# Optimization experiments

Measured on AMD Instinct MI355X. Metric: run time of the kernel, lower is better.

Reference implementation:

```python
import jax, jax.numpy as jnp
import numpy as np

I = 256  # input size
H = 256  # hidden size
B = 128
S = 1024
EPS = 1e-5


def setup_inputs() -> dict:
    key = jax.random.key(0)
    ks = jax.random.split(key, 8)
    bound = 1.0 / np.sqrt(H)
    x = jax.random.normal(ks[0], (B, S, I), dtype=jnp.float32)
    mask = jax.random.randint(ks[1], (B, S), 0, 2) == 1
    W_ih = jax.random.uniform(ks[2], (4 * H, I), jnp.float32, -bound, bound)
    W_hh = jax.random.uniform(ks[3], (4 * H, H), jnp.float32, -bound, bound)
    b_ih = jax.random.uniform(ks[4], (4 * H,), jnp.float32, -bound, bound)
    b_hh = jax.random.uniform(ks[5], (4 * H,), jnp.float32, -bound, bound)
    gamma = jnp.ones((H,), jnp.float32)
    beta = jnp.zeros((H,), jnp.float32)
    return {"x": x, "mask": mask, "W_ih": W_ih, "W_hh": W_hh,
            "b_ih": b_ih, "b_hh": b_hh, "gamma": gamma, "beta": beta}


def _layernorm(h, gamma, beta):
    mu = jnp.mean(h, axis=-1, keepdims=True)
    var = jnp.var(h, axis=-1, keepdims=True)
    return (h - mu) * jax.lax.rsqrt(var + EPS) * gamma + beta


def reference(x, mask, W_ih, W_hh, b_ih, b_hh, gamma, beta):
    b = x.shape[0]
    h0 = jnp.zeros((b, H), x.dtype)
    c0 = jnp.zeros((b, H), x.dtype)
    out0 = jnp.zeros((b, H), x.dtype)

    def step(carry, inp):
        h, c, out = carry
        x_t, m_t = inp  # (B,I), (B,)
        hn = _layernorm(h, gamma, beta)
        gates = x_t @ W_ih.T + b_ih + hn @ W_hh.T + b_hh  # (B,4H)
        i_g, f_g, g_g, o_g = jnp.split(gates, 4, axis=-1)
        c = jax.nn.sigmoid(f_g) * c + jax.nn.sigmoid(i_g) * jnp.tanh(g_g)
        h = jax.nn.sigmoid(o_g) * jnp.tanh(c)
        # output[~mask] = h[~mask]; where mask is True the old output is kept
        out = jnp.where(m_t[:, None], out, h)
        return (h, c, out), None

    xs = (jnp.swapaxes(x, 0, 1), jnp.swapaxes(mask, 0, 1))  # (S,B,I), (S,B)
    (h, c, out), _ = jax.lax.scan(step, (h0, c0, out0), xs)
    return out
```

## Files before the change

kernel.cpp:

```cpp
#include <hip/hip_runtime.h>
#include <hip/hip_bf16.h>
#include <stdint.h>


#define Bb 128
#define Ss 1024
#define Ii 256
#define Hh 256
#define G4v 1024
#define EPSF 1e-5f

typedef __bf16 bf16;
typedef _Float16 f16;
typedef __attribute__((ext_vector_type(8))) __bf16 bf16x8;
typedef __attribute__((ext_vector_type(4))) __bf16 bf16x4;
typedef __attribute__((ext_vector_type(8))) _Float16 f16x8;
typedef __attribute__((ext_vector_type(4))) _Float16 f16x4;
typedef __attribute__((ext_vector_type(4))) float f32x4;
typedef unsigned int u32;
typedef unsigned long long u64;

static __device__ __forceinline__ f32x4 mfma16b(bf16x8 a, bf16x8 b, f32x4 c) {
  return __builtin_amdgcn_mfma_f32_16x16x32_bf16(a, b, c, 0, 0, 0);
}
static __device__ __forceinline__ f32x4 mfma16h(f16x8 a, f16x8 b, f32x4 c) {
  return __builtin_amdgcn_mfma_f32_16x16x32_f16(a, b, c, 0, 0, 0);
}
static __device__ __forceinline__ float sigm(float x) { return 1.0f / (1.0f + __expf(-x)); }
static __device__ __forceinline__ float tanhf_(float x) {
  float e = __expf(-2.0f * fabsf(x));
  float t = (1.0f - e) / (1.0f + e);
  return x < 0.0f ? -t : t;
}
static __device__ __forceinline__ unsigned short ush(f16 h) {
  return __builtin_bit_cast(unsigned short, h);
}
static __device__ __forceinline__ f16 hus(unsigned short u) {
  return __builtin_bit_cast(f16, u);
}

__global__ void k_conv_wih(const float* __restrict__ W, bf16* __restrict__ hi,
                           bf16* __restrict__ lo) {
  int i = (blockIdx.x * 256 + threadIdx.x) * 4;
  f32x4 v = *(const f32x4*)(W + i);
  bf16x4 h_, l_;
#pragma unroll
  for (int j = 0; j < 4; ++j) {
    bf16 hh = (bf16)v[j];
    h_[j] = hh;
    l_[j] = (bf16)(v[j] - (float)hh);
  }
  *(bf16x4*)(hi + i) = h_;
  *(bf16x4*)(lo + i) = l_;
}

__global__ void k_prep_whh(const float* __restrict__ W, const float* __restrict__ gamma,
                           f16* __restrict__ Wf) {
  int tid = blockIdx.x * 256 + threadIdx.x;
  int lane = tid & 63;
  int fk = tid >> 6;
  int ntg = fk >> 3, kt = fk & 7;
  int g = ntg * 16 + (lane & 15);
  int k = kt * 32 + ((lane >> 4) << 3);
  f16x8 r;
#pragma unroll
  for (int j = 0; j < 8; ++j) r[j] = (f16)(W[g * Hh + k + j] * gamma[k + j]);
  *(f16x8*)(Wf + (size_t)tid * 8) = r;
}

__global__ void k_prep_rd(const float* __restrict__ W, const float* __restrict__ gamma,
                          const float* __restrict__ beta, const float* __restrict__ bih,
                          const float* __restrict__ bhh, float* __restrict__ RD) {
  int g = blockIdx.x * 256 + threadIdx.x;
  float r = 0.f, d = 0.f;
  for (int k = 0; k < Hh; ++k) {
    float w = W[g * Hh + k];
    r += w * gamma[k];
    d += w * beta[k];
  }
  RD[2 * g] = r;
  RD[2 * g + 1] = d + bih[g] + bhh[g];
}

__global__ __launch_bounds__(256, 2) void k_gemm(const float* __restrict__ x,
                                                 const bf16* __restrict__ Whi,
                                                 const bf16* __restrict__ Wlo,
                                                 float* __restrict__ xw,
                                                 int t0, int Tc, int ntb) {
  __shared__ bf16 Bs[2][128 * 128];
  int bid = blockIdx.x;
  int b = bid & 127;
  int r2 = bid >> 7;
  int tb = r2 % ntb;
  int gt = r2 / ntb;
  int g0 = gt * 128;
  int tid = threadIdx.x, w = tid >> 6, lane = tid & 63;
  int li = lane & 15, lg = lane >> 4;
  char* BsB = (char*)Bs;
  int tbase = tb * 128 + 32 * w;
  f32x4 acc[2][8];
#pragma unroll
  for (int mt = 0; mt < 2; ++mt)
#pragma unroll
    for (int nt = 0; nt < 8; ++nt) acc[mt][nt] = (f32x4){0.f, 0.f, 0.f, 0.f};

  for (int kp = 0; kp < 2; ++kp) {
#pragma unroll
    for (int it = 0; it < 8; ++it) {
      int p = it * 4096 + tid * 16;
      int row = p >> 8, colb = p & 255;
      size_t goff = (size_t)(g0 + row) * 512 + kp * 256 + colb;
      int dst = row * 256 + (colb ^ ((row & 7) << 4));
      *(bf16x8*)(BsB + dst) = *(const bf16x8*)((const char*)Whi + goff);
      *(bf16x8*)(BsB + 32768 + dst) = *(const bf16x8*)((const char*)Wlo + goff);
    }
    __syncthreads();
#pragma unroll
    for (int kt = 0; kt < 4; ++kt) {
      int kl = kt * 32 + lg * 8;
      int kgl = kp * 128 + kl;
      bf16x8 ah[2], al[2];
#pragma unroll
      for (int mt = 0; mt < 2; ++mt) {
        int t = t0 + tbase + 16 * mt + li;
        const float* xp = x + ((size_t)b * Ss + t) * Ii + kgl;
        f32x4 f0 = *(const f32x4*)xp;
        f32x4 f1 = *(const f32x4*)(xp + 4);
        bf16x8 hv, lv;
#pragma unroll
        for (int j = 0; j < 4; ++j) {
          bf16 h0 = (bf16)f0[j];
          hv[j] = h0;
          lv[j] = (bf16)(f0[j] - (float)h0);
          bf16 h1 = (bf16)f1[j];
          hv[4 + j] = h1;
          lv[4 + j] = (bf16)(f1[j] - (float)h1);
        }
        ah[mt] = hv;
        al[mt] = lv;
      }
#pragma unroll
      for (int nt = 0; nt < 8; ++nt) {
        int grow = nt * 16 + li;
        int off = grow * 256 + ((kl * 2) ^ ((grow & 7) << 4));
        bf16x8 bh = *(const bf16x8*)(BsB + off);
        bf16x8 bl = *(const bf16x8*)(BsB + 32768 + off);
#pragma unroll
        for (int mt = 0; mt < 2; ++mt) {
          acc[mt][nt] = mfma16b(ah[mt], bh, acc[mt][nt]);
          acc[mt][nt] = mfma16b(ah[mt], bl, acc[mt][nt]);
          acc[mt][nt] = mfma16b(al[mt], bh, acc[mt][nt]);
        }
      }
    }
    __syncthreads();
  }
#pragma unroll
  for (int mt = 0; mt < 2; ++mt)
#pragma unroll
    for (int nt = 0; nt < 8; ++nt)
#pragma unroll
      for (int r = 0; r < 4; ++r) {
        int tl = tbase + 16 * mt + lg * 4 + r;
        int g = g0 + nt * 16 + li;
        xw[((size_t)b * Tc + tl) * G4v + g] = acc[mt][nt][r];
      }
}

__global__ __launch_bounds__(256, 1) void k_recur(
    const f16* __restrict__ Wf, const float* __restrict__ xw,
    const int* __restrict__ mask, const float* __restrict__ RD,
    float* __restrict__ st_h, float* __restrict__ st_c, float* __restrict__ st_o,
    u64* pub, float* __restrict__ out, int t0, int Tc, int first, int last) {
  __shared__ f16 hb[2][16 * 256];
  __shared__ float murs[2][16][2];
  __shared__ float2 spw[4][16];
  __shared__ float spart[16][16][2];
  int bid = blockIdx.x;
  int grp = bid & 7, q = bid >> 3;
  int tid = threadIdx.x, w = tid >> 6, lane = tid & 63;
  int li = lane & 15, lg = lane >> 4;
  int b0 = grp * 16;
  int jloc = (q * 4 + w) * 16 + li;
  char* hbB = (char*)hb;

  f16x8 wp[4][8];
#pragma unroll
  for (int c = 0; c < 4; ++c)
#pragma unroll
    for (int kt = 0; kt < 8; ++kt) {
      int ntg = c * 16 + q * 4 + w;
      wp[c][kt] = *(const f16x8*)(Wf + ((size_t)(ntg * 8 + kt) * 64 + lane) * 8);
      asm volatile("" : "+a"(wp[c][kt]));
    }
  float Rr[4], Dd[4];
#pragma unroll
  for (int c = 0; c < 4; ++c) {
    int g = c * 256 + jloc;
    Rr[c] = RD[2 * g];
    Dd[c] = RD[2 * g + 1];
  }

  float cst[4], ost[4];
  if (first) {
#pragma unroll
    for (int i = 0; i < 16; ++i) {
      hb[0][tid * 16 + i] = (f16)0.0f;
      hb[1][tid * 16 + i] = (f16)0.0f;
    }
#pragma unroll
    for (int r = 0; r < 4; ++r) { cst[r] = 0.f; ost[r] = 0.f; }
    if (tid < 16) { murs[0][tid][0] = 0.f; murs[0][tid][1] = rsqrtf(EPSF); }
  } else {
    int row = tid >> 4, cs = tid & 15, jseg = cs * 16;
    float s = 0.f, ss = 0.f;
#pragma unroll
    for (int i = 0; i < 16; ++i) {
      float v = st_h[(size_t)(b0 + row) * Hh + jseg + i];
      s += v;
      ss += v * v;
      f16 hh = (f16)v;
      int boff = row * 512 + (((jseg + i) * 2) ^ ((row & 7) << 4));
      *(f16*)(hbB + boff) = hh;
      *(f16*)(hbB + 8192 + boff) = (f16)(v - (float)hh);
    }
    spart[row][cs][0] = s;
    spart[row][cs][1] = ss;
#pragma unroll
    for (int r = 0; r < 4; ++r) {
      int m = lg * 4 + r;
      cst[r] = st_c[(size_t)(b0 + m) * Hh + jloc];
      ost[r] = st_o[(size_t)(b0 + m) * Hh + jloc];
    }
    __syncthreads();
    if (tid < 16) {
      float s2 = 0.f, ss2 = 0.f;
#pragma unroll
      for (int i = 0; i < 16; ++i) { s2 += spart[tid][i][0]; ss2 += spart[tid][i][1]; }
      float mu = s2 * (1.f / 256.f);
      float var = ss2 * (1.f / 256.f) - mu * mu;
      float rs = rsqrtf(var + EPSF);
      murs[0][tid][0] = mu * rs;
      murs[0][tid][1] = rs;
    }
  }
  __syncthreads();

  float xwv[4][4];
  int mk[4];
#pragma unroll
  for (int c = 0; c < 4; ++c)
#pragma unroll
    for (int r = 0; r < 4; ++r)
      xwv[c][r] = xw[((size_t)(b0 + lg * 4 + r) * Tc + 0) * G4v + c * 256 + jloc];
#pragma unroll
  for (int r = 0; r < 4; ++r) mk[r] = mask[(size_t)(b0 + lg * 4 + r) * Ss + t0];

  int grow = tid >> 4, gcg = tid & 15;

  for (int tl = 0; tl < Tc; ++tl) {
    int tg = t0 + tl;
    int slot = (tg + 1) & 1;
    u32 want = (u32)(tg + 1);

    f32x4 a0[4], a1[4];
#pragma unroll
    for (int c = 0; c < 4; ++c) {
      a0[c] = (f32x4){0.f, 0.f, 0.f, 0.f};
      a1[c] = (f32x4){0.f, 0.f, 0.f, 0.f};
    }
#pragma unroll
    for (int kt = 0; kt < 8; ++kt) {
      int aoff = li * 512 + (((kt * 32 + lg * 8) * 2) ^ ((li & 7) << 4));
      f16x8 ah = *(const f16x8*)(hbB + aoff);
      f16x8 al = *(const f16x8*)(hbB + 8192 + aoff);
#pragma unroll
      for (int c = 0; c < 4; ++c) {
        a0[c] = mfma16h(ah, wp[c][kt], a0[c]);
        a1[c] = mfma16h(al, wp[c][kt], a1[c]);
      }
    }
    float mrs[4], rsv[4];
#pragma unroll
    for (int r = 0; r < 4; ++r) {
      int m = lg * 4 + r;
      mrs[r] = murs[tl & 1][m][0];
      rsv[r] = murs[tl & 1][m][1];
    }
    __syncthreads();

    float hnew[4];
#pragma unroll
    for (int r = 0; r < 4; ++r) {
      float i_ = (a0[0][r] + a1[0][r]) * rsv[r] - mrs[r] * Rr[0] + Dd[0] + xwv[0][r];
      float f_ = (a0[1][r] + a1[1][r]) * rsv[r] - mrs[r] * Rr[1] + Dd[1] + xwv[1][r];
      float g_ = (a0[2][r] + a1[2][r]) * rsv[r] - mrs[r] * Rr[2] + Dd[2] + xwv[2][r];
      float o_ = (a0[3][r] + a1[3][r]) * rsv[r] - mrs[r] * Rr[3] + Dd[3] + xwv[3][r];
      float cn = sigm(f_) * cst[r] + sigm(i_) * tanhf_(g_);
      float hn = sigm(o_) * tanhf_(cn);
      cst[r] = cn;
      ost[r] = mk[r] ? ost[r] : hn;
      hnew[r] = hn;
    }
    u64* ph = pub + (size_t)(slot * 32 + bid) * 1024;
#pragma unroll
    for (int r = 0; r < 4; ++r) {
      int m = lg * 4 + r;
      float hn = hnew[r];
      f16 hh = (f16)hn;
      f16 hl = (f16)(hn - (float)hh);
      int boff = m * 512 + ((jloc * 2) ^ ((m & 7) << 4));
      *(f16*)(hbB + boff) = hh;
      *(f16*)(hbB + 8192 + boff) = hl;
      u64 pv = ((u64)want << 32) | ((u32)ush(hh) << 16) | (u32)ush(hl);
      __hip_atomic_store(&ph[m * 64 + (w * 16 + li)], pv, __ATOMIC_RELAXED,
                         __HIP_MEMORY_SCOPE_AGENT);
    }

    u64 gv[3][4];
    const u64* srcs[3];
#pragma unroll
    for (int pi = 0; pi < 3; ++pi) {
      int qq = (q + 1 + pi) & 3;
      int pbid = qq * 8 + grp;
      srcs[pi] = pub + (size_t)(slot * 32 + pbid) * 1024 + grow * 64 + gcg * 4;
#pragma unroll
      for (int e = 0; e < 4; ++e)
        gv[pi][e] = __hip_atomic_load(&srcs[pi][e], __ATOMIC_RELAXED,
                                      __HIP_MEMORY_SCOPE_AGENT);
    }

    {
      float sr[4], qr[4];
#pragma unroll
      for (int r = 0; r < 4; ++r) { sr[r] = hnew[r]; qr[r] = hnew[r] * hnew[r]; }
#pragma unroll
      for (int msk = 1; msk < 16; msk <<= 1)
#pragma unroll
        for (int r = 0; r < 4; ++r) {
          sr[r] += __shfl_xor(sr[r], msk);
          qr[r] += __shfl_xor(qr[r], msk);
        }
      if (li == 0)
#pragma unroll
        for (int r = 0; r < 4; ++r) spw[w][lg * 4 + r] = make_float2(sr[r], qr[r]);
    }
    if (tl == Tc - 1) {
#pragma unroll
      for (int r = 0; r < 4; ++r) {
        int m = lg * 4 + r;
        st_h[(size_t)(b0 + m) * Hh + jloc] = hnew[r];
        st_c[(size_t)(b0 + m) * Hh + jloc] = cst[r];
        st_o[(size_t)(b0 + m) * Hh + jloc] = ost[r];
      }
      if (last) {
#pragma unroll
        for (int r = 0; r < 4; ++r) out[(size_t)(b0 + lg * 4 + r) * Hh + jloc] = ost[r];
      }
    }
    {
      int tln = (tl + 1 < Tc) ? tl + 1 : Tc - 1;
#pragma unroll
      for (int c = 0; c < 4; ++c)
#pragma unroll
        for (int r = 0; r < 4; ++r)
          xwv[c][r] = xw[((size_t)(b0 + lg * 4 + r) * Tc + tln) * G4v + c * 256 + jloc];
#pragma unroll
      for (int r = 0; r < 4; ++r) mk[r] = mask[(size_t)(b0 + lg * 4 + r) * Ss + t0 + tln];
    }

    {
      u32 bad = 0;
#pragma unroll
      for (int pi = 0; pi < 3; ++pi)
#pragma unroll
        for (int e = 0; e < 4; ++e) bad |= (u32)(gv[pi][e] >> 32) ^ want;
      int cnt = 0;
      while (bad) {
#pragma unroll
        for (int pi = 0; pi < 3; ++pi)
#pragma unroll
          for (int e = 0; e < 4; ++e)
            gv[pi][e] = __hip_atomic_load(&srcs[pi][e], __ATOMIC_RELAXED,
                                          __HIP_MEMORY_SCOPE_AGENT);
        bad = 0;
#pragma unroll
        for (int pi = 0; pi < 3; ++pi)
#pragma unroll
          for (int e = 0; e < 4; ++e) bad |= (u32)(gv[pi][e] >> 32) ^ want;
        if (++cnt > (1 << 20)) break;
      }
    }
    float su = 0.f, qu = 0.f;
#pragma unroll
    for (int pi = 0; pi < 3; ++pi) {
      int qq = (q + 1 + pi) & 3;
      int j0 = qq * 64 + gcg * 4;
      int boff = grow * 512 + ((j0 * 2) ^ ((grow & 7) << 4));
      f16x4 h4, l4;
#pragma unroll
      for (int e = 0; e < 4; ++e) {
        u32 d = (u32)gv[pi][e];
        f16 hh = hus((unsigned short)(d >> 16));
        f16 hl = hus((unsigned short)(d & 0xffffu));
        h4[e] = hh;
        l4[e] = hl;
        float f = (float)hh + (float)hl;
        su += f;
        qu += f * f;
      }
      *(f16x4*)(hbB + boff) = h4;
      *(f16x4*)(hbB + 8192 + boff) = l4;
    }
#pragma unroll
    for (int msk = 1; msk < 16; msk <<= 1) {
      su += __shfl_xor(su, msk);
      qu += __shfl_xor(qu, msk);
    }
    __syncthreads();
    if (li == 0) {
      float s = su + spw[0][grow].x + spw[1][grow].x + spw[2][grow].x + spw[3][grow].x;
      float ss2 = qu + spw[0][grow].y + spw[1][grow].y + spw[2][grow].y + spw[3][grow].y;
      float mu = s * (1.f / 256.f);
      float var = ss2 * (1.f / 256.f) - mu * mu;
      float rs = rsqrtf(var + EPSF);
      murs[(tl + 1) & 1][grow][0] = mu * rs;
      murs[(tl + 1) & 1][grow][1] = rs;
    }
  }
}

extern "C" void kernel_launch(void* const* d_in, const int* in_sizes, int n_in,
                              void* d_out, int out_size, void* d_ws, size_t ws_size,
                              hipStream_t stream) {
  (void)in_sizes; (void)n_in; (void)out_size;
  const float* x = (const float*)d_in[0];
  const int* mask = (const int*)d_in[1];
  const float* Wih = (const float*)d_in[2];
  const float* Whh = (const float*)d_in[3];
  const float* bih = (const float*)d_in[4];
  const float* bhh = (const float*)d_in[5];
  const float* gamma = (const float*)d_in[6];
  const float* beta = (const float*)d_in[7];
  float* outp = (float*)d_out;
  char* ws = (char*)d_ws;

  const size_t extra = 3 * (512u << 10) + (8u << 10) + 3 * (128u << 10) +
                       (512u << 10) + (64u << 10);
  int Tc = 128;
  if (ws_size >= (size_t)1024 * 524288 + extra) Tc = 1024;
  else if (ws_size >= (size_t)512 * 524288 + extra) Tc = 512;
  else if (ws_size >= (size_t)256 * 524288 + extra) Tc = 256;

  size_t o = 0;
  auto take = [&](size_t bytes) { size_t r = o; o += (bytes + 255) & ~(size_t)255; return r; };
  size_t xw_off = take((size_t)Bb * Tc * G4v * 4);
  size_t wihh_off = take(512u << 10);
  size_t wihl_off = take(512u << 10);
  size_t whh_off = take(512u << 10);
  size_t rd_off = take(8u << 10);
  size_t sth_off = take(128u << 10);
  size_t stc_off = take(128u << 10);
  size_t sto_off = take(128u << 10);
  size_t pub_off = take(512u << 10);

  bf16* wihh = (bf16*)(ws + wihh_off);
  bf16* wihl = (bf16*)(ws + wihl_off);
  f16* whhf = (f16*)(ws + whh_off);
  float* rd = (float*)(ws + rd_off);
  float* xwp = (float*)(ws + xw_off);
  float* sth = (float*)(ws + sth_off);
  float* stc = (float*)(ws + stc_off);
  float* sto = (float*)(ws + sto_off);
  u64* pubh = (u64*)(ws + pub_off);

  hipMemsetAsync(pubh, 0, 512u << 10, stream);
  k_conv_wih<<<dim3(256), dim3(256), 0, stream>>>(Wih, wihh, wihl);
  k_prep_whh<<<dim3(128), dim3(256), 0, stream>>>(Whh, gamma, whhf);
  k_prep_rd<<<dim3(4), dim3(256), 0, stream>>>(Whh, gamma, beta, bih, bhh, rd);

  int nchunk = Ss / Tc;
  int ntb = Tc / 128;
  for (int ci = 0; ci < nchunk; ++ci) {
    int t0 = ci * Tc;
    k_gemm<<<dim3(8 * ntb * 128), dim3(256), 0, stream>>>(x, wihh, wihl, xwp, t0, Tc, ntb);
    k_recur<<<dim3(32), dim3(256), 0, stream>>>(whhf, xwp, mask, rd, sth, stc, sto,
                                                pubh, outp, t0, Tc,
                                                ci == 0 ? 1 : 0, ci == nchunk - 1 ? 1 : 0);
  }
}
```

Baseline: 4.757 ms.

## Give each recurrent block a full hidden slice, removing cross-block spin synchronization

The recurrence now runs on 8 workgroups, each owning 16 batch rows and all 256 hidden units. Previously 32 workgroups split the hidden dimension and exchanged h every step through atomic publish/poll in global memory, with a spin wait. Now each step needs only block-local barriers and LDS. Each workgroup does four times the MFMA work per step, so the recurrent weights are split three ways: half held in registers, a quarter staged in dynamic LDS, and a quarter re-read from global/L2 every step. This trades per-step inter-block latency for more per-block compute and weight traffic.

```diff
diff --git a/kernel.cpp b/kernel.cpp
--- a/kernel.cpp
+++ b/kernel.cpp
@@ -10,15 +10,21 @@
 #define G4v 1024
 #define EPSF 1e-5f
 
+#define OFF_W 0
+#define OFF_HBH 131072
+#define OFF_HBL 139264
+#define OFF_RD 147456
+#define OFF_MURS 155648
+#define OFF_SPW 155904
+#define OFF_SPART 156416
+#define LDS_TOTAL 158464
+
 typedef __bf16 bf16;
 typedef _Float16 f16;
 typedef __attribute__((ext_vector_type(8))) __bf16 bf16x8;
-typedef __attribute__((ext_vector_type(4))) __bf16 bf16x4;
 typedef __attribute__((ext_vector_type(8))) _Float16 f16x8;
-typedef __attribute__((ext_vector_type(4))) _Float16 f16x4;
 typedef __attribute__((ext_vector_type(4))) float f32x4;
 typedef unsigned int u32;
-typedef unsigned long long u64;
 
 static __device__ __forceinline__ f32x4 mfma16b(bf16x8 a, bf16x8 b, f32x4 c) {
   return __builtin_amdgcn_mfma_f32_16x16x32_bf16(a, b, c, 0, 0, 0);
@@ -32,26 +38,17 @@
   float t = (1.0f - e) / (1.0f + e);
   return x < 0.0f ? -t : t;
 }
-static __device__ __forceinline__ unsigned short ush(f16 h) {
-  return __builtin_bit_cast(unsigned short, h);
-}
-static __device__ __forceinline__ f16 hus(unsigned short u) {
-  return __builtin_bit_cast(f16, u);
-}
 
 __global__ void k_conv_wih(const float* __restrict__ W, bf16* __restrict__ hi,
                            bf16* __restrict__ lo) {
   int i = (blockIdx.x * 256 + threadIdx.x) * 4;
   f32x4 v = *(const f32x4*)(W + i);
-  bf16x4 h_, l_;
 #pragma unroll
   for (int j = 0; j < 4; ++j) {
     bf16 hh = (bf16)v[j];
-    h_[j] = hh;
-    l_[j] = (bf16)(v[j] - (float)hh);
-  }
-  *(bf16x4*)(hi + i) = h_;
-  *(bf16x4*)(lo + i) = l_;
+    hi[i + j] = hh;
+    lo[i + j] = (bf16)(v[j] - (float)hh);
+  }
 }
 
 __global__ void k_prep_whh(const float* __restrict__ W, const float* __restrict__ gamma,
@@ -171,46 +168,58 @@
     const f16* __restrict__ Wf, const float* __restrict__ xw,
     const int* __restrict__ mask, const float* __restrict__ RD,
     float* __restrict__ st_h, float* __restrict__ st_c, float* __restrict__ st_o,
-    u64* pub, float* __restrict__ out, int t0, int Tc, int first, int last) {
-  __shared__ f16 hb[2][16 * 256];
-  __shared__ float murs[2][16][2];
-  __shared__ float2 spw[4][16];
-  __shared__ float spart[16][16][2];
+    float* __restrict__ out, int t0, int Tc, int first, int last) {
+  extern __shared__ char smem[];
+  char* WldsB = smem + OFF_W;
+  char* hbH = smem + OFF_HBH;
+  char* hbL = smem + OFF_HBL;
+  float* rdl = (float*)(smem + OFF_RD);
+  float(*murs)[16][2] = (float(*)[16][2])(smem + OFF_MURS);
+  float2(*spw)[16] = (float2(*)[16])(smem + OFF_SPW);
+  float(*spart)[16][2] = (float(*)[16][2])(smem + OFF_SPART);
+
   int bid = blockIdx.x;
-  int grp = bid & 7, q = bid >> 3;
   int tid = threadIdx.x, w = tid >> 6, lane = tid & 63;
   int li = lane & 15, lg = lane >> 4;
-  int b0 = grp * 16;
-  int jloc = (q * 4 + w) * 16 + li;
-  char* hbB = (char*)hb;
-
-  f16x8 wp[4][8];
+  int b0 = bid * 16;
+
+  f16x8 wp[2][4][8];
+#pragma unroll
+  for (int jt = 0; jt < 2; ++jt)
+#pragma unroll
+    for (int c = 0; c < 4; ++c)
+#pragma unroll
+      for (int kt = 0; kt < 8; ++kt) {
+        int ntg = c * 16 + (w * 4 + jt);
+        wp[jt][c][kt] = *(const f16x8*)(Wf + ((size_t)(ntg * 8 + kt) * 64 + lane) * 8);
+        asm volatile("" : "+a"(wp[jt][c][kt]));
+      }
 #pragma unroll
   for (int c = 0; c < 4; ++c)
 #pragma unroll
     for (int kt = 0; kt < 8; ++kt) {
-      int ntg = c * 16 + q * 4 + w;
-      wp[c][kt] = *(const f16x8*)(Wf + ((size_t)(ntg * 8 + kt) * 64 + lane) * 8);
-      asm volatile("" : "+a"(wp[c][kt]));
-    }
-  float Rr[4], Dd[4];
-#pragma unroll
-  for (int c = 0; c < 4; ++c) {
-    int g = c * 256 + jloc;
-    Rr[c] = RD[2 * g];
-    Dd[c] = RD[2 * g + 1];
-  }
-
-  float cst[4], ost[4];
+      int ntg = c * 16 + (w * 4 + 2);
+      f16x8 v = *(const f16x8*)(Wf + ((size_t)(ntg * 8 + kt) * 64 + lane) * 8);
+      *(f16x8*)(WldsB + (size_t)((w * 32 + c * 8 + kt) * 64 + lane) * 16) = v;
+    }
+  *(f32x4*)(rdl + tid * 8) = *(const f32x4*)(RD + tid * 8);
+  *(f32x4*)(rdl + tid * 8 + 4) = *(const f32x4*)(RD + tid * 8 + 4);
+
+  float cst[4][4], ost[4][4];
   if (first) {
 #pragma unroll
     for (int i = 0; i < 16; ++i) {
-      hb[0][tid * 16 + i] = (f16)0.0f;
-      hb[1][tid * 16 + i] = (f16)0.0f;
-    }
-#pragma unroll
-    for (int r = 0; r < 4; ++r) { cst[r] = 0.f; ost[r] = 0.f; }
-    if (tid < 16) { murs[0][tid][0] = 0.f; murs[0][tid][1] = rsqrtf(EPSF); }
+      ((f16*)hbH)[tid * 16 + i] = (f16)0.0f;
+      ((f16*)hbL)[tid * 16 + i] = (f16)0.0f;
+    }
+#pragma unroll
+    for (int jt = 0; jt < 4; ++jt)
+#pragma unroll
+      for (int r = 0; r < 4; ++r) { cst[jt][r] = 0.f; ost[jt][r] = 0.f; }
+    if (tid < 16) {
+      murs[0][tid][0] = 0.f;
+      murs[0][tid][1] = rsqrtf(EPSF);
+    }
   } else {
     int row = tid >> 4, cs = tid & 15, jseg = cs * 16;
     float s = 0.f, ss = 0.f;
@@ -221,16 +230,20 @@
       ss += v * v;
       f16 hh = (f16)v;
       int boff = row * 512 + (((jseg + i) * 2) ^ ((row & 7) << 4));
-      *(f16*)(hbB + boff) = hh;
-      *(f16*)(hbB + 8192 + boff) = (f16)(v - (float)hh);
+      *(f16*)(hbH + boff) = hh;
+      *(f16*)(hbL + boff) = (f16)(v - (float)hh);
     }
     spart[row][cs][0] = s;
     spart[row][cs][1] = ss;
 #pragma unroll
-    for (int r = 0; r < 4; ++r) {
-      int m = lg * 4 + r;
-      cst[r] = st_c[(size_t)(b0 + m) * Hh + jloc];
-      ost[r] = st_o[(size_t)(b0 + m) * Hh + jloc];
+    for (int jt = 0; jt < 4; ++jt) {
+      int jloc = (w * 4 + jt) * 16 + li;
+#pragma unroll
+      for (int r = 0; r < 4; ++r) {
+        int m = lg * 4 + r;
+        cst[jt][r] = st_c[(size_t)(b0 + m) * Hh + jloc];
+        ost[jt][r] = st_o[(size_t)(b0 + m) * Hh + jloc];
+      }
     }
     __syncthreads();
     if (tid < 16) {
@@ -246,40 +259,39 @@
   }
   __syncthreads();
 
-  float xwv[4][4];
   int mk[4];
 #pragma unroll
-  for (int c = 0; c < 4; ++c)
-#pragma unroll
-    for (int r = 0; r < 4; ++r)
-      xwv[c][r] = xw[((size_t)(b0 + lg * 4 + r) * Tc + 0) * G4v + c * 256 + jloc];
-#pragma unroll
   for (int r = 0; r < 4; ++r) mk[r] = mask[(size_t)(b0 + lg * 4 + r) * Ss + t0];
 
-  int grow = tid >> 4, gcg = tid & 15;
-
   for (int tl = 0; tl < Tc; ++tl) {
-    int tg = t0 + tl;
-    int slot = (tg + 1) & 1;
-    u32 want = (u32)(tg + 1);
-
-    f32x4 a0[4], a1[4];
-#pragma unroll
-    for (int c = 0; c < 4; ++c) {
-      a0[c] = (f32x4){0.f, 0.f, 0.f, 0.f};
-      a1[c] = (f32x4){0.f, 0.f, 0.f, 0.f};
-    }
+    f16x8 ah[8], al[8];
 #pragma unroll
     for (int kt = 0; kt < 8; ++kt) {
       int aoff = li * 512 + (((kt * 32 + lg * 8) * 2) ^ ((li & 7) << 4));
-      f16x8 ah = *(const f16x8*)(hbB + aoff);
-      f16x8 al = *(const f16x8*)(hbB + 8192 + aoff);
-#pragma unroll
-      for (int c = 0; c < 4; ++c) {
-        a0[c] = mfma16h(ah, wp[c][kt], a0[c]);
-        a1[c] = mfma16h(al, wp[c][kt], a1[c]);
-      }
-    }
+      ah[kt] = *(const f16x8*)(hbH + aoff);
+      al[kt] = *(const f16x8*)(hbL + aoff);
+    }
+    float xwc[4][4];
+    {
+      int jl0 = (w * 4) * 16 + li;
+#pragma unroll
+      for (int c = 0; c < 4; ++c)
+#pragma unroll
+        for (int r = 0; r < 4; ++r)
+          xwc[c][r] = xw[((size_t)(b0 + lg * 4 + r) * Tc + tl) * G4v + c * 256 + jl0];
+    }
+    f16x8 wsA[8], wsB[8];
+#pragma unroll
+    for (int kt = 0; kt < 8; ++kt) {
+      int ntg = 0 * 16 + (w * 4 + 3);
+      wsA[kt] = *(const f16x8*)(Wf + ((size_t)(ntg * 8 + kt) * 64 + lane) * 8);
+    }
+    int tln = (tl + 1 < Tc) ? tl + 1 : Tc - 1;
+    int mkn[4];
+#pragma unroll
+    for (int r = 0; r < 4; ++r) mkn[r] = mask[(size_t)(b0 + lg * 4 + r) * Ss + t0 + tln];
+
+    __syncthreads();
     float mrs[4], rsv[4];
 #pragma unroll
     for (int r = 0; r < 4; ++r) {
@@ -287,145 +299,124 @@
       mrs[r] = murs[tl & 1][m][0];
       rsv[r] = murs[tl & 1][m][1];
     }
+    float sr[4] = {0.f, 0.f, 0.f, 0.f}, qr[4] = {0.f, 0.f, 0.f, 0.f};
+    int lastStep = (tl == Tc - 1);
+
+#pragma unroll
+    for (int jt = 0; jt < 4; ++jt) {
+      int jloc = (w * 4 + jt) * 16 + li;
+      float xwn[4][4];
+      if (jt < 3) {
+        int jln = (w * 4 + jt + 1) * 16 + li;
+#pragma unroll
+        for (int c = 0; c < 4; ++c)
+#pragma unroll
+          for (int r = 0; r < 4; ++r)
+            xwn[c][r] = xw[((size_t)(b0 + lg * 4 + r) * Tc + tl) * G4v + c * 256 + jln];
+      }
+      f32x4 acc[4];
+#pragma unroll
+      for (int c = 0; c < 4; ++c) acc[c] = (f32x4){0.f, 0.f, 0.f, 0.f};
+      if (jt < 2) {
+#pragma unroll
+        for (int c = 0; c < 4; ++c)
+#pragma unroll
+          for (int kt = 0; kt < 8; ++kt) {
+            acc[c] = mfma16h(ah[kt], wp[jt][c][kt], acc[c]);
+            acc[c] = mfma16h(al[kt], wp[jt][c][kt], acc[c]);
+          }
+      } else if (jt == 2) {
+#pragma unroll
+        for (int c = 0; c < 4; ++c) {
+          f16x8 wl[8];
+#pragma unroll
+          for (int kt = 0; kt < 8; ++kt)
+            wl[kt] = *(const f16x8*)(WldsB +
+                                     (size_t)((w * 32 + c * 8 + kt) * 64 + lane) * 16);
+#pragma unroll
+          for (int kt = 0; kt < 8; ++kt) {
+            acc[c] = mfma16h(ah[kt], wl[kt], acc[c]);
+            acc[c] = mfma16h(al[kt], wl[kt], acc[c]);
+          }
+        }
+      } else {
+#pragma unroll
+        for (int c = 0; c < 4; ++c) {
+          if (c < 3) {
+            int ntg = (c + 1) * 16 + (w * 4 + 3);
+#pragma unroll
+            for (int kt = 0; kt < 8; ++kt) {
+              f16x8 v = *(const f16x8*)(Wf + ((size_t)(ntg * 8 + kt) * 64 + lane) * 8);
+              if (c & 1) wsA[kt] = v; else wsB[kt] = v;
+            }
+          }
+#pragma unroll
+          for (int kt = 0; kt < 8; ++kt) {
+            f16x8 wc = (c & 1) ? wsB[kt] : wsA[kt];
+            acc[c] = mfma16h(ah[kt], wc, acc[c]);
+            acc[c] = mfma16h(al[kt], wc, acc[c]);
+          }
+        }
+      }
+      float Rrc[4], Ddc[4];
+#pragma unroll
+      for (int c = 0; c < 4; ++c) {
+        int g = c * 256 + jloc;
+        Rrc[c] = rdl[2 * g];
+        Ddc[c] = rdl[2 * g + 1];
+      }
+#pragma unroll
+      for (int r = 0; r < 4; ++r) {
+        float i_ = acc[0][r] * rsv[r] - mrs[r] * Rrc[0] + Ddc[0] + xwc[0][r];
+        float f_ = acc[1][r] * rsv[r] - mrs[r] * Rrc[1] + Ddc[1] + xwc[1][r];
+        float g_ = acc[2][r] * rsv[r] - mrs[r] * Rrc[2] + Ddc[2] + xwc[2][r];
+        float o_ = acc[3][r] * rsv[r] - mrs[r] * Rrc[3] + Ddc[3] + xwc[3][r];
+        float cn = sigm(f_) * cst[jt][r] + sigm(i_) * tanhf_(g_);
+        float hn = sigm(o_) * tanhf_(cn);
+        cst[jt][r] = cn;
+        ost[jt][r] = mk[r] ? ost[jt][r] : hn;
+        int m = lg * 4 + r;
+        int boff = m * 512 + ((jloc * 2) ^ ((m & 7) << 4));
+        f16 hh = (f16)hn;
+        *(f16*)(hbH + boff) = hh;
+        *(f16*)(hbL + boff) = (f16)(hn - (float)hh);
+        sr[r] += hn;
+        qr[r] += hn * hn;
+        if (lastStep) {
+          st_h[(size_t)(b0 + m) * Hh + jloc] = hn;
+          st_c[(size_t)(b0 + m) * Hh + jloc] = cst[jt][r];
+          st_o[(size_t)(b0 + m) * Hh + jloc] = ost[jt][r];
+          if (last) out[(size_t)(b0 + m) * Hh + jloc] = ost[jt][r];
+        }
+      }
+      if (jt < 3) {
+#pragma unroll
+        for (int c = 0; c < 4; ++c)
+#pragma unroll
+          for (int r = 0; r < 4; ++r) xwc[c][r] = xwn[c][r];
+      }
+    }
+#pragma unroll
+    for (int msk = 1; msk < 16; msk <<= 1)
+#pragma unroll
+      for (int r = 0; r < 4; ++r) {
+        sr[r] += __shfl_xor(sr[r], msk);
+        qr[r] += __shfl_xor(qr[r], msk);
+      }
+    if (li == 0)
+#pragma unroll
+      for (int r = 0; r < 4; ++r) spw[w][lg * 4 + r] = make_float2(sr[r], qr[r]);
+#pragma unroll
+    for (int r = 0; r < 4; ++r) mk[r] = mkn[r];
     __syncthreads();
-
-    float hnew[4];
-#pragma unroll
-    for (int r = 0; r < 4; ++r) {
-      float i_ = (a0[0][r] + a1[0][r]) * rsv[r] - mrs[r] * Rr[0] + Dd[0] + xwv[0][r];
-      float f_ = (a0[1][r] + a1[1][r]) * rsv[r] - mrs[r] * Rr[1] + Dd[1] + xwv[1][r];
-      float g_ = (a0[2][r] + a1[2][r]) * rsv[r] - mrs[r] * Rr[2] + Dd[2] + xwv[2][r];
-      float o_ = (a0[3][r] + a1[3][r]) * rsv[r] - mrs[r] * Rr[3] + Dd[3] + xwv[3][r];
-      float cn = sigm(f_) * cst[r] + sigm(i_) * tanhf_(g_);
-      float hn = sigm(o_) * tanhf_(cn);
-      cst[r] = cn;
-      ost[r] = mk[r] ? ost[r] : hn;
-      hnew[r] = hn;
-    }
-    u64* ph = pub + (size_t)(slot * 32 + bid) * 1024;
-#pragma unroll
-    for (int r = 0; r < 4; ++r) {
-      int m = lg * 4 + r;
-      float hn = hnew[r];
-      f16 hh = (f16)hn;
-      f16 hl = (f16)(hn - (float)hh);
-      int boff = m * 512 + ((jloc * 2) ^ ((m & 7) << 4));
-      *(f16*)(hbB + boff) = hh;
-      *(f16*)(hbB + 8192 + boff) = hl;
-      u64 pv = ((u64)want << 32) | ((u32)ush(hh) << 16) | (u32)ush(hl);
-      __hip_atomic_store(&ph[m * 64 + (w * 16 + li)], pv, __ATOMIC_RELAXED,
-                         __HIP_MEMORY_SCOPE_AGENT);
-    }
-
-    u64 gv[3][4];
-    const u64* srcs[3];
-#pragma unroll
-    for (int pi = 0; pi < 3; ++pi) {
-      int qq = (q + 1 + pi) & 3;
-      int pbid = qq * 8 + grp;
-      srcs[pi] = pub + (size_t)(slot * 32 + pbid) * 1024 + grow * 64 + gcg * 4;
-#pragma unroll
-      for (int e = 0; e < 4; ++e)
-        gv[pi][e] = __hip_atomic_load(&srcs[pi][e], __ATOMIC_RELAXED,
-                                      __HIP_MEMORY_SCOPE_AGENT);
-    }
-
-    {
-      float sr[4], qr[4];
-#pragma unroll
-      for (int r = 0; r < 4; ++r) { sr[r] = hnew[r]; qr[r] = hnew[r] * hnew[r]; }
-#pragma unroll
-      for (int msk = 1; msk < 16; msk <<= 1)
-#pragma unroll
-        for (int r = 0; r < 4; ++r) {
-          sr[r] += __shfl_xor(sr[r], msk);
-          qr[r] += __shfl_xor(qr[r], msk);
-        }
-      if (li == 0)
-#pragma unroll
-        for (int r = 0; r < 4; ++r) spw[w][lg * 4 + r] = make_float2(sr[r], qr[r]);
-    }
-    if (tl == Tc - 1) {
-#pragma unroll
-      for (int r = 0; r < 4; ++r) {
-        int m = lg * 4 + r;
-        st_h[(size_t)(b0 + m) * Hh + jloc] = hnew[r];
-        st_c[(size_t)(b0 + m) * Hh + jloc] = cst[r];
-        st_o[(size_t)(b0 + m) * Hh + jloc] = ost[r];
-      }
-      if (last) {
-#pragma unroll
-        for (int r = 0; r < 4; ++r) out[(size_t)(b0 + lg * 4 + r) * Hh + jloc] = ost[r];
-      }
-    }
-    {
-      int tln = (tl + 1 < Tc) ? tl + 1 : Tc - 1;
-#pragma unroll
-      for (int c = 0; c < 4; ++c)
-#pragma unroll
-        for (int r = 0; r < 4; ++r)
-          xwv[c][r] = xw[((size_t)(b0 + lg * 4 + r) * Tc + tln) * G4v + c * 256 + jloc];
-#pragma unroll
-      for (int r = 0; r < 4; ++r) mk[r] = mask[(size_t)(b0 + lg * 4 + r) * Ss + t0 + tln];
-    }
-
-    {
-      u32 bad = 0;
-#pragma unroll
-      for (int pi = 0; pi < 3; ++pi)
-#pragma unroll
-        for (int e = 0; e < 4; ++e) bad |= (u32)(gv[pi][e] >> 32) ^ want;
-      int cnt = 0;
-      while (bad) {
-#pragma unroll
-        for (int pi = 0; pi < 3; ++pi)
-#pragma unroll
-          for (int e = 0; e < 4; ++e)
-            gv[pi][e] = __hip_atomic_load(&srcs[pi][e], __ATOMIC_RELAXED,
-                                          __HIP_MEMORY_SCOPE_AGENT);
-        bad = 0;
-#pragma unroll
-        for (int pi = 0; pi < 3; ++pi)
-#pragma unroll
-          for (int e = 0; e < 4; ++e) bad |= (u32)(gv[pi][e] >> 32) ^ want;
-        if (++cnt > (1 << 20)) break;
-      }
-    }
-    float su = 0.f, qu = 0.f;
-#pragma unroll
-    for (int pi = 0; pi < 3; ++pi) {
-      int qq = (q + 1 + pi) & 3;
-      int j0 = qq * 64 + gcg * 4;
-      int boff = grow * 512 + ((j0 * 2) ^ ((grow & 7) << 4));
-      f16x4 h4, l4;
-#pragma unroll
-      for (int e = 0; e < 4; ++e) {
-        u32 d = (u32)gv[pi][e];
-        f16 hh = hus((unsigned short)(d >> 16));
-        f16 hl = hus((unsigned short)(d & 0xffffu));
-        h4[e] = hh;
-        l4[e] = hl;
-        float f = (float)hh + (float)hl;
-        su += f;
-        qu += f * f;
-      }
-      *(f16x4*)(hbB + boff) = h4;
-      *(f16x4*)(hbB + 8192 + boff) = l4;
-    }
-#pragma unroll
-    for (int msk = 1; msk < 16; msk <<= 1) {
-      su += __shfl_xor(su, msk);
-      qu += __shfl_xor(qu, msk);
-    }
-    __syncthreads();
-    if (li == 0) {
-      float s = su + spw[0][grow].x + spw[1][grow].x + spw[2][grow].x + spw[3][grow].x;
-      float ss2 = qu + spw[0][grow].y + spw[1][grow].y + spw[2][grow].y + spw[3][grow].y;
+    if (tid < 16) {
+      float s = spw[0][tid].x + spw[1][tid].x + spw[2][tid].x + spw[3][tid].x;
+      float ss2 = spw[0][tid].y + spw[1][tid].y + spw[2][tid].y + spw[3][tid].y;
       float mu = s * (1.f / 256.f);
       float var = ss2 * (1.f / 256.f) - mu * mu;
       float rs = rsqrtf(var + EPSF);
-      murs[(tl + 1) & 1][grow][0] = mu * rs;
-      murs[(tl + 1) & 1][grow][1] = rs;
+      murs[(tl + 1) & 1][tid][0] = mu * rs;
+      murs[(tl + 1) & 1][tid][1] = rs;
     }
   }
 }
@@ -445,8 +436,14 @@
   float* outp = (float*)d_out;
   char* ws = (char*)d_ws;
 
-  const size_t extra = 3 * (512u << 10) + (8u << 10) + 3 * (128u << 10) +
-                       (512u << 10) + (64u << 10);
+  static int lds_set = 0;
+  if (!lds_set) {
+    hipFuncSetAttribute((const void*)k_recur,
+                        hipFuncAttributeMaxDynamicSharedMemorySize, LDS_TOTAL);
+    lds_set = 1;
+  }
+
+  const size_t extra = 3 * (512u << 10) + (8u << 10) + 3 * (128u << 10) + (64u << 10);
   int Tc = 128;
   if (ws_size >= (size_t)1024 * 524288 + extra) Tc = 1024;
   else if (ws_size >= (size_t)512 * 524288 + extra) Tc = 512;
@@ -462,7 +459,6 @@
   size_t sth_off = take(128u << 10);
   size_t stc_off = take(128u << 10);
   size_t sto_off = take(128u << 10);
-  size_t pub_off = take(512u << 10);
 
   bf16* wihh = (bf16*)(ws + wihh_off);
   bf16* wihl = (bf16*)(ws + wihl_off);
@@ -472,9 +468,7 @@
   float* sth = (float*)(ws + sth_off);
   float* stc = (float*)(ws + stc_off);
   float* sto = (float*)(ws + sto_off);
-  u64* pubh = (u64*)(ws + pub_off);
-
-  hipMemsetAsync(pubh, 0, 512u << 10, stream);
+
   k_conv_wih<<<dim3(256), dim3(256), 0, stream>>>(Wih, wihh, wihl);
   k_prep_whh<<<dim3(128), dim3(256), 0, stream>>>(Whh, gamma, whhf);
   k_prep_rd<<<dim3(4), dim3(256), 0, stream>>>(Whh, gamma, beta, bih, bhh, rd);
@@ -484,8 +478,8 @@
   for (int ci = 0; ci < nchunk; ++ci) {
     int t0 = ci * Tc;
     k_gemm<<<dim3(8 * ntb * 128), dim3(256), 0, stream>>>(x, wihh, wihl, xwp, t0, Tc, ntb);
-    k_recur<<<dim3(32), dim3(256), 0, stream>>>(whhf, xwp, mask, rd, sth, stc, sto,
-                                                pubh, outp, t0, Tc,
-                                                ci == 0 ? 1 : 0, ci == nchunk - 1 ? 1 : 0);
-  }
-}
+    k_recur<<<dim3(8), dim3(256), LDS_TOTAL, stream>>>(whhf, xwp, mask, rd, sth, stc, sto,
+                                                       outp, t0, Tc,
+                                                       ci == 0 ? 1 : 0, ci == nchunk - 1 ? 1 : 0);
+  }
+}
```

After: 15.27 ms. 221% more time.

## Split recurrence across 16 blocks with pairwise hidden-state exchange

Applied to the files above, without the earlier changes.

The recurrent kernel now runs on 16 workgroups instead of 32. Each block owns 128 hidden units for a 16-row batch group and exchanges its half of h with a single partner block instead of three peers. This cuts per-step cross-block polling and publish traffic, and each wave now issues twice as many MFMAs from register-resident weights. The cost is more weight registers per wave, fewer CUs on the serial critical path, and an extra barrier per step. The bf16 weight conversion kernel also switches from vector stores to scalar stores.

```diff
diff --git a/kernel.cpp b/kernel.cpp
--- a/kernel.cpp
+++ b/kernel.cpp
@@ -13,9 +13,7 @@
 typedef __bf16 bf16;
 typedef _Float16 f16;
 typedef __attribute__((ext_vector_type(8))) __bf16 bf16x8;
-typedef __attribute__((ext_vector_type(4))) __bf16 bf16x4;
 typedef __attribute__((ext_vector_type(8))) _Float16 f16x8;
-typedef __attribute__((ext_vector_type(4))) _Float16 f16x4;
 typedef __attribute__((ext_vector_type(4))) float f32x4;
 typedef unsigned int u32;
 typedef unsigned long long u64;
@@ -43,15 +41,12 @@
                            bf16* __restrict__ lo) {
   int i = (blockIdx.x * 256 + threadIdx.x) * 4;
   f32x4 v = *(const f32x4*)(W + i);
-  bf16x4 h_, l_;
 #pragma unroll
   for (int j = 0; j < 4; ++j) {
     bf16 hh = (bf16)v[j];
-    h_[j] = hh;
-    l_[j] = (bf16)(v[j] - (float)hh);
-  }
-  *(bf16x4*)(hi + i) = h_;
-  *(bf16x4*)(lo + i) = l_;
+    hi[i + j] = hh;
+    lo[i + j] = (bf16)(v[j] - (float)hh);
+  }
 }
 
 __global__ void k_prep_whh(const float* __restrict__ W, const float* __restrict__ gamma,
@@ -172,44 +167,54 @@
     const int* __restrict__ mask, const float* __restrict__ RD,
     float* __restrict__ st_h, float* __restrict__ st_c, float* __restrict__ st_o,
     u64* pub, float* __restrict__ out, int t0, int Tc, int first, int last) {
-  __shared__ f16 hb[2][16 * 256];
+  __shared__ f16 hbH[16 * 256];
+  __shared__ f16 hbL[16 * 256];
   __shared__ float murs[2][16][2];
   __shared__ float2 spw[4][16];
+  __shared__ float2 sprem[16];
   __shared__ float spart[16][16][2];
   int bid = blockIdx.x;
-  int grp = bid & 7, q = bid >> 3;
+  int grp = bid & 7, half = bid >> 3;
   int tid = threadIdx.x, w = tid >> 6, lane = tid & 63;
   int li = lane & 15, lg = lane >> 4;
   int b0 = grp * 16;
-  int jloc = (q * 4 + w) * 16 + li;
-  char* hbB = (char*)hb;
-
-  f16x8 wp[4][8];
-#pragma unroll
-  for (int c = 0; c < 4; ++c)
-#pragma unroll
-    for (int kt = 0; kt < 8; ++kt) {
-      int ntg = c * 16 + q * 4 + w;
-      wp[c][kt] = *(const f16x8*)(Wf + ((size_t)(ntg * 8 + kt) * 64 + lane) * 8);
-      asm volatile("" : "+a"(wp[c][kt]));
-    }
-  float Rr[4], Dd[4];
-#pragma unroll
-  for (int c = 0; c < 4; ++c) {
-    int g = c * 256 + jloc;
-    Rr[c] = RD[2 * g];
-    Dd[c] = RD[2 * g + 1];
-  }
-
-  float cst[4], ost[4];
+  char* hbHB = (char*)hbH;
+  char* hbLB = (char*)hbL;
+
+  f16x8 wp[2][4][8];
+#pragma unroll
+  for (int jt = 0; jt < 2; ++jt)
+#pragma unroll
+    for (int c = 0; c < 4; ++c)
+#pragma unroll
+      for (int kt = 0; kt < 8; ++kt) {
+        int ntg = c * 16 + (half * 8 + w * 2 + jt);
+        wp[jt][c][kt] = *(const f16x8*)(Wf + ((size_t)(ntg * 8 + kt) * 64 + lane) * 8);
+        asm volatile("" : "+a"(wp[jt][c][kt]));
+      }
+  int jloc0 = half * 128 + (w * 2) * 16 + li;
+  int jloc1 = jloc0 + 16;
+  float Rr[2][4], Dd[2][4];
+#pragma unroll
+  for (int jt = 0; jt < 2; ++jt)
+#pragma unroll
+    for (int c = 0; c < 4; ++c) {
+      int g = c * 256 + (jt ? jloc1 : jloc0);
+      Rr[jt][c] = RD[2 * g];
+      Dd[jt][c] = RD[2 * g + 1];
+    }
+
+  float cst[2][4], ost[2][4];
   if (first) {
 #pragma unroll
     for (int i = 0; i < 16; ++i) {
-      hb[0][tid * 16 + i] = (f16)0.0f;
-      hb[1][tid * 16 + i] = (f16)0.0f;
-    }
-#pragma unroll
-    for (int r = 0; r < 4; ++r) { cst[r] = 0.f; ost[r] = 0.f; }
+      hbH[tid * 16 + i] = (f16)0.0f;
+      hbL[tid * 16 + i] = (f16)0.0f;
+    }
+#pragma unroll
+    for (int jt = 0; jt < 2; ++jt)
+#pragma unroll
+      for (int r = 0; r < 4; ++r) { cst[jt][r] = 0.f; ost[jt][r] = 0.f; }
     if (tid < 16) { murs[0][tid][0] = 0.f; murs[0][tid][1] = rsqrtf(EPSF); }
   } else {
     int row = tid >> 4, cs = tid & 15, jseg = cs * 16;
@@ -221,16 +226,20 @@
       ss += v * v;
       f16 hh = (f16)v;
       int boff = row * 512 + (((jseg + i) * 2) ^ ((row & 7) << 4));
-      *(f16*)(hbB + boff) = hh;
-      *(f16*)(hbB + 8192 + boff) = (f16)(v - (float)hh);
+      *(f16*)(hbHB + boff) = hh;
+      *(f16*)(hbLB + boff) = (f16)(v - (float)hh);
     }
     spart[row][cs][0] = s;
     spart[row][cs][1] = ss;
 #pragma unroll
-    for (int r = 0; r < 4; ++r) {
-      int m = lg * 4 + r;
-      cst[r] = st_c[(size_t)(b0 + m) * Hh + jloc];
-      ost[r] = st_o[(size_t)(b0 + m) * Hh + jloc];
+    for (int jt = 0; jt < 2; ++jt) {
+      int jl = jt ? jloc1 : jloc0;
+#pragma unroll
+      for (int r = 0; r < 4; ++r) {
+        int m = lg * 4 + r;
+        cst[jt][r] = st_c[(size_t)(b0 + m) * Hh + jl];
+        ost[jt][r] = st_o[(size_t)(b0 + m) * Hh + jl];
+      }
     }
     __syncthreads();
     if (tid < 16) {
@@ -246,40 +255,50 @@
   }
   __syncthreads();
 
-  float xwv[4][4];
+  float xwv[2][4][4];
   int mk[4];
 #pragma unroll
-  for (int c = 0; c < 4; ++c)
-#pragma unroll
-    for (int r = 0; r < 4; ++r)
-      xwv[c][r] = xw[((size_t)(b0 + lg * 4 + r) * Tc + 0) * G4v + c * 256 + jloc];
+  for (int jt = 0; jt < 2; ++jt) {
+    int jl = jt ? jloc1 : jloc0;
+#pragma unroll
+    for (int c = 0; c < 4; ++c)
+#pragma unroll
+      for (int r = 0; r < 4; ++r)
+        xwv[jt][c][r] = xw[((size_t)(b0 + lg * 4 + r) * Tc + 0) * G4v + c * 256 + jl];
+  }
 #pragma unroll
   for (int r = 0; r < 4; ++r) mk[r] = mask[(size_t)(b0 + lg * 4 + r) * Ss + t0];
 
   int grow = tid >> 4, gcg = tid & 15;
+  int phalf = half ^ 1;
+  int pbid = bid ^ 8;
 
   for (int tl = 0; tl < Tc; ++tl) {
     int tg = t0 + tl;
     int slot = (tg + 1) & 1;
     u32 want = (u32)(tg + 1);
 
-    f32x4 a0[4], a1[4];
-#pragma unroll
-    for (int c = 0; c < 4; ++c) {
-      a0[c] = (f32x4){0.f, 0.f, 0.f, 0.f};
-      a1[c] = (f32x4){0.f, 0.f, 0.f, 0.f};
-    }
+    f16x8 ah[8], al[8];
 #pragma unroll
     for (int kt = 0; kt < 8; ++kt) {
       int aoff = li * 512 + (((kt * 32 + lg * 8) * 2) ^ ((li & 7) << 4));
-      f16x8 ah = *(const f16x8*)(hbB + aoff);
-      f16x8 al = *(const f16x8*)(hbB + 8192 + aoff);
-#pragma unroll
-      for (int c = 0; c < 4; ++c) {
-        a0[c] = mfma16h(ah, wp[c][kt], a0[c]);
-        a1[c] = mfma16h(al, wp[c][kt], a1[c]);
-      }
-    }
+      ah[kt] = *(const f16x8*)(hbHB + aoff);
+      al[kt] = *(const f16x8*)(hbLB + aoff);
+    }
+    f32x4 acc[2][4];
+#pragma unroll
+    for (int jt = 0; jt < 2; ++jt)
+#pragma unroll
+      for (int c = 0; c < 4; ++c) acc[jt][c] = (f32x4){0.f, 0.f, 0.f, 0.f};
+#pragma unroll
+    for (int kt = 0; kt < 8; ++kt)
+#pragma unroll
+      for (int jt = 0; jt < 2; ++jt)
+#pragma unroll
+        for (int c = 0; c < 4; ++c) {
+          acc[jt][c] = mfma16h(ah[kt], wp[jt][c][kt], acc[jt][c]);
+          acc[jt][c] = mfma16h(al[kt], wp[jt][c][kt], acc[jt][c]);
+        }
     float mrs[4], rsv[4];
 #pragma unroll
     for (int r = 0; r < 4; ++r) {
@@ -289,82 +308,81 @@
     }
     __syncthreads();
 
-    float hnew[4];
-#pragma unroll
-    for (int r = 0; r < 4; ++r) {
-      float i_ = (a0[0][r] + a1[0][r]) * rsv[r] - mrs[r] * Rr[0] + Dd[0] + xwv[0][r];
-      float f_ = (a0[1][r] + a1[1][r]) * rsv[r] - mrs[r] * Rr[1] + Dd[1] + xwv[1][r];
-      float g_ = (a0[2][r] + a1[2][r]) * rsv[r] - mrs[r] * Rr[2] + Dd[2] + xwv[2][r];
-      float o_ = (a0[3][r] + a1[3][r]) * rsv[r] - mrs[r] * Rr[3] + Dd[3] + xwv[3][r];
-      float cn = sigm(f_) * cst[r] + sigm(i_) * tanhf_(g_);
-      float hn = sigm(o_) * tanhf_(cn);
-      cst[r] = cn;
-      ost[r] = mk[r] ? ost[r] : hn;
-      hnew[r] = hn;
-    }
-    u64* ph = pub + (size_t)(slot * 32 + bid) * 1024;
-#pragma unroll
-    for (int r = 0; r < 4; ++r) {
-      int m = lg * 4 + r;
-      float hn = hnew[r];
-      f16 hh = (f16)hn;
-      f16 hl = (f16)(hn - (float)hh);
-      int boff = m * 512 + ((jloc * 2) ^ ((m & 7) << 4));
-      *(f16*)(hbB + boff) = hh;
-      *(f16*)(hbB + 8192 + boff) = hl;
-      u64 pv = ((u64)want << 32) | ((u32)ush(hh) << 16) | (u32)ush(hl);
-      __hip_atomic_store(&ph[m * 64 + (w * 16 + li)], pv, __ATOMIC_RELAXED,
-                         __HIP_MEMORY_SCOPE_AGENT);
-    }
-
-    u64 gv[3][4];
-    const u64* srcs[3];
-#pragma unroll
-    for (int pi = 0; pi < 3; ++pi) {
-      int qq = (q + 1 + pi) & 3;
-      int pbid = qq * 8 + grp;
-      srcs[pi] = pub + (size_t)(slot * 32 + pbid) * 1024 + grow * 64 + gcg * 4;
-#pragma unroll
-      for (int e = 0; e < 4; ++e)
-        gv[pi][e] = __hip_atomic_load(&srcs[pi][e], __ATOMIC_RELAXED,
-                                      __HIP_MEMORY_SCOPE_AGENT);
-    }
-
-    {
-      float sr[4], qr[4];
-#pragma unroll
-      for (int r = 0; r < 4; ++r) { sr[r] = hnew[r]; qr[r] = hnew[r] * hnew[r]; }
-#pragma unroll
-      for (int msk = 1; msk < 16; msk <<= 1)
+    float sr[4] = {0.f, 0.f, 0.f, 0.f}, qr[4] = {0.f, 0.f, 0.f, 0.f};
+    float hnS[2][4];
+    u64* ph = pub + (size_t)(slot * 16 + bid) * 2048;
+#pragma unroll
+    for (int jt = 0; jt < 2; ++jt) {
+      int jl = jt ? jloc1 : jloc0;
+      int loc = jl - half * 128;
+#pragma unroll
+      for (int r = 0; r < 4; ++r) {
+        float i_ = acc[jt][0][r] * rsv[r] - mrs[r] * Rr[jt][0] + Dd[jt][0] + xwv[jt][0][r];
+        float f_ = acc[jt][1][r] * rsv[r] - mrs[r] * Rr[jt][1] + Dd[jt][1] + xwv[jt][1][r];
+        float g_ = acc[jt][2][r] * rsv[r] - mrs[r] * Rr[jt][2] + Dd[jt][2] + xwv[jt][2][r];
+        float o_ = acc[jt][3][r] * rsv[r] - mrs[r] * Rr[jt][3] + Dd[jt][3] + xwv[jt][3][r];
+        float cn = sigm(f_) * cst[jt][r] + sigm(i_) * tanhf_(g_);
+        float hn = sigm(o_) * tanhf_(cn);
+        cst[jt][r] = cn;
+        ost[jt][r] = mk[r] ? ost[jt][r] : hn;
+        hnS[jt][r] = hn;
+        int m = lg * 4 + r;
+        f16 hh = (f16)hn;
+        f16 hl = (f16)(hn - (float)hh);
+        int boff = m * 512 + ((jl * 2) ^ ((m & 7) << 4));
+        *(f16*)(hbHB + boff) = hh;
+        *(f16*)(hbLB + boff) = hl;
+        u64 pv = ((u64)want << 32) | ((u32)ush(hh) << 16) | (u32)ush(hl);
+        __hip_atomic_store(&ph[m * 128 + loc], pv, __ATOMIC_RELAXED,
+                           __HIP_MEMORY_SCOPE_AGENT);
+        sr[r] += hn;
+        qr[r] += hn * hn;
+      }
+    }
+
+    const u64* src = pub + (size_t)(slot * 16 + pbid) * 2048 + grow * 128 + gcg * 8;
+    u64 gv[8];
+#pragma unroll
+    for (int e = 0; e < 8; ++e)
+      gv[e] = __hip_atomic_load(&src[e], __ATOMIC_RELAXED, __HIP_MEMORY_SCOPE_AGENT);
+
+#pragma unroll
+    for (int msk = 1; msk < 16; msk <<= 1)
+#pragma unroll
+      for (int r = 0; r < 4; ++r) {
+        sr[r] += __shfl_xor(sr[r], msk);
+        qr[r] += __shfl_xor(qr[r], msk);
+      }
+    if (li == 0)
+#pragma unroll
+      for (int r = 0; r < 4; ++r) spw[w][lg * 4 + r] = make_float2(sr[r], qr[r]);
+
+    if (tl == Tc - 1) {
+#pragma unroll
+      for (int jt = 0; jt < 2; ++jt) {
+        int jl = jt ? jloc1 : jloc0;
 #pragma unroll
         for (int r = 0; r < 4; ++r) {
-          sr[r] += __shfl_xor(sr[r], msk);
-          qr[r] += __shfl_xor(qr[r], msk);
+          int m = lg * 4 + r;
+          st_h[(size_t)(b0 + m) * Hh + jl] = hnS[jt][r];
+          st_c[(size_t)(b0 + m) * Hh + jl] = cst[jt][r];
+          st_o[(size_t)(b0 + m) * Hh + jl] = ost[jt][r];
+          if (last) out[(size_t)(b0 + m) * Hh + jl] = ost[jt][r];
         }
-      if (li == 0)
-#pragma unroll
-        for (int r = 0; r < 4; ++r) spw[w][lg * 4 + r] = make_float2(sr[r], qr[r]);
-    }
-    if (tl == Tc - 1) {
-#pragma unroll
-      for (int r = 0; r < 4; ++r) {
-        int m = lg * 4 + r;
-        st_h[(size_t)(b0 + m) * Hh + jloc] = hnew[r];
-        st_c[(size_t)(b0 + m) * Hh + jloc] = cst[r];
-        st_o[(size_t)(b0 + m) * Hh + jloc] = ost[r];
-      }
-      if (last) {
-#pragma unroll
-        for (int r = 0; r < 4; ++r) out[(size_t)(b0 + lg * 4 + r) * Hh + jloc] = ost[r];
       }
     }
     {
       int tln = (tl + 1 < Tc) ? tl + 1 : Tc - 1;
 #pragma unroll
-      for (int c = 0; c < 4; ++c)
-#pragma unroll
-        for (int r = 0; r < 4; ++r)
-          xwv[c][r] = xw[((size_t)(b0 + lg * 4 + r) * Tc + tln) * G4v + c * 256 + jloc];
+      for (int jt = 0; jt < 2; ++jt) {
+        int jl = jt ? jloc1 : jloc0;
+#pragma unroll
+        for (int c = 0; c < 4; ++c)
+#pragma unroll
+          for (int r = 0; r < 4; ++r)
+            xwv[jt][c][r] =
+                xw[((size_t)(b0 + lg * 4 + r) * Tc + tln) * G4v + c * 256 + jl];
+      }
 #pragma unroll
       for (int r = 0; r < 4; ++r) mk[r] = mask[(size_t)(b0 + lg * 4 + r) * Ss + t0 + tln];
     }
@@ -372,61 +390,56 @@
     {
       u32 bad = 0;
 #pragma unroll
-      for (int pi = 0; pi < 3; ++pi)
-#pragma unroll
-        for (int e = 0; e < 4; ++e) bad |= (u32)(gv[pi][e] >> 32) ^ want;
+      for (int e = 0; e < 8; ++e) bad |= (u32)(gv[e] >> 32) ^ want;
       int cnt = 0;
       while (bad) {
 #pragma unroll
-        for (int pi = 0; pi < 3; ++pi)
-#pragma unroll
-          for (int e = 0; e < 4; ++e)
-            gv[pi][e] = __hip_atomic_load(&srcs[pi][e], __ATOMIC_RELAXED,
-                                          __HIP_MEMORY_SCOPE_AGENT);
+        for (int e = 0; e < 8; ++e)
+          gv[e] = __hip_atomic_load(&src[e], __ATOMIC_RELAXED, __HIP_MEMORY_SCOPE_AGENT);
         bad = 0;
 #pragma unroll
-        for (int pi = 0; pi < 3; ++pi)
-#pragma unroll
-          for (int e = 0; e < 4; ++e) bad |= (u32)(gv[pi][e] >> 32) ^ want;
+        for (int e = 0; e < 8; ++e) bad |= (u32)(gv[e] >> 32) ^ want;
         if (++cnt > (1 << 20)) break;
       }
     }
-    float su = 0.f, qu = 0.f;
-#pragma unroll
-    for (int pi = 0; pi < 3; ++pi) {
-      int qq = (q + 1 + pi) & 3;
-      int j0 = qq * 64 + gcg * 4;
+    {
+      int j0 = phalf * 128 + gcg * 8;
       int boff = grow * 512 + ((j0 * 2) ^ ((grow & 7) << 4));
-      f16x4 h4, l4;
-#pragma unroll
-      for (int e = 0; e < 4; ++e) {
-        u32 d = (u32)gv[pi][e];
+      f16x8 h8, l8;
+      float su = 0.f, qu = 0.f;
+#pragma unroll
+      for (int e = 0; e < 8; ++e) {
+        u32 d = (u32)gv[e];
         f16 hh = hus((unsigned short)(d >> 16));
         f16 hl = hus((unsigned short)(d & 0xffffu));
-        h4[e] = hh;
-        l4[e] = hl;
+        h8[e] = hh;
+        l8[e] = hl;
         float f = (float)hh + (float)hl;
         su += f;
         qu += f * f;
       }
-      *(f16x4*)(hbB + boff) = h4;
-      *(f16x4*)(hbB + 8192 + boff) = l4;
-    }
-#pragma unroll
-    for (int msk = 1; msk < 16; msk <<= 1) {
-      su += __shfl_xor(su, msk);
-      qu += __shfl_xor(qu, msk);
+      *(f16x8*)(hbHB + boff) = h8;
+      *(f16x8*)(hbLB + boff) = l8;
+#pragma unroll
+      for (int msk = 1; msk < 16; msk <<= 1) {
+        su += __shfl_xor(su, msk);
+        qu += __shfl_xor(qu, msk);
+      }
+      if (li == 0) sprem[grow] = make_float2(su, qu);
     }
     __syncthreads();
-    if (li == 0) {
-      float s = su + spw[0][grow].x + spw[1][grow].x + spw[2][grow].x + spw[3][grow].x;
-      float ss2 = qu + spw[0][grow].y + spw[1][grow].y + spw[2][grow].y + spw[3][grow].y;
+    if (tid < 16) {
+      float s = sprem[tid].x + spw[0][tid].x + spw[1][tid].x + spw[2][tid].x +
+                spw[3][tid].x;
+      float ss2 = sprem[tid].y + spw[0][tid].y + spw[1][tid].y + spw[2][tid].y +
+                  spw[3][tid].y;
       float mu = s * (1.f / 256.f);
       float var = ss2 * (1.f / 256.f) - mu * mu;
       float rs = rsqrtf(var + EPSF);
-      murs[(tl + 1) & 1][grow][0] = mu * rs;
-      murs[(tl + 1) & 1][grow][1] = rs;
-    }
+      murs[(tl + 1) & 1][tid][0] = mu * rs;
+      murs[(tl + 1) & 1][tid][1] = rs;
+    }
+    __syncthreads();
   }
 }
 
@@ -484,7 +497,7 @@
   for (int ci = 0; ci < nchunk; ++ci) {
     int t0 = ci * Tc;
     k_gemm<<<dim3(8 * ntb * 128), dim3(256), 0, stream>>>(x, wihh, wihl, xwp, t0, Tc, ntb);
-    k_recur<<<dim3(32), dim3(256), 0, stream>>>(whhf, xwp, mask, rd, sth, stc, sto,
+    k_recur<<<dim3(16), dim3(256), 0, stream>>>(whhf, xwp, mask, rd, sth, stc, sto,
                                                 pubh, outp, t0, Tc,
                                                 ci == 0 ? 1 : 0, ci == nchunk - 1 ? 1 : 0);
   }
```

After: 6.077 ms. 27.8% more time.
